# Kernel tuning notes

Measured on AMD Instinct MI355X. Metric: run time of the kernel, lower is better.

The kernel has to match this reference:

```python
import jax, jax.numpy as jnp
import numpy as np

B, S, H = 1, 4096, 2048
NH, HD = 16, 128  # num_heads, head_dim = H // NH


def setup_inputs() -> dict:
    key = jax.random.key(0)
    k1, k2, k3 = jax.random.split(key, 3)
    x = jax.random.normal(k1, (B, S, H), dtype=jnp.float32)
    w_qkv = jax.random.normal(k2, (3 * H, H), dtype=jnp.float32) * (1.0 / np.sqrt(H))
    w_out = jax.random.normal(k3, (H, H), dtype=jnp.float32) * (1.0 / np.sqrt(H))
    return {"x": x, "w_qkv": w_qkv, "w_out": w_out}


def reference(x, w_qkv, w_out):
    b, s, _ = x.shape
    # qkv projection: torch Linear computes x @ W^T
    qkv = jnp.einsum('bsh,oh->bso', x, w_qkv)
    qkv = qkv.reshape(b, s, 3, NH, HD).transpose(2, 0, 3, 1, 4)  # [3,B,NH,S,HD]
    q, k, v = qkv[0], qkv[1], qkv[2]
    # world_size == 1 -> single ring step == full attention with online softmax
    scores = jnp.einsum('bhqd,bhkd->bhqk', q, k) / np.sqrt(HD)
    m = jnp.max(scores, axis=-1, keepdims=True)          # running max (single step)
    p = jnp.exp(scores - m)                              # scores_exp
    out = jnp.einsum('bhqk,bhkd->bhqd', p, v)
    denom = jnp.sum(p, axis=-1, keepdims=True) + 1e-8    # running_sum + eps
    out = out / denom
    out = out.transpose(0, 2, 1, 3).reshape(b, s, H)     # [B,S,H]
    return jnp.einsum('bsh,oh->bso', out, w_out)
```

## Files before the change

kernel.cpp:

```cpp
#include <hip/hip_runtime.h>
#include <stdint.h>

typedef __attribute__((ext_vector_type(4))) float f32x4;
typedef __attribute__((ext_vector_type(16))) float f32x16;
typedef __attribute__((ext_vector_type(8))) short bf16x8;
typedef unsigned short u16;

#define MFMA(a, b, c) __builtin_amdgcn_mfma_f32_16x16x32_bf16(a, b, c, 0, 0, 0)
#define MFMA32(a, b, c) __builtin_amdgcn_mfma_f32_32x32x16_bf16(a, b, c, 0, 0, 0)
#define EXP2(x) __builtin_amdgcn_exp2f(x)
#define FENCE asm volatile("" ::: "memory")
#define BARRIER do { FENCE; __builtin_amdgcn_s_barrier(); FENCE; } while (0)

__device__ __forceinline__ u16 f2bf(float f) {
  union { float f; unsigned u; } x; x.f = f;
  unsigned r = x.u + 0x7fffu + ((x.u >> 16) & 1u);
  return (u16)(r >> 16);
}

__device__ __forceinline__ unsigned cvtpk(float lo, float hi) {
  unsigned r;
  asm("v_cvt_pk_bf16_f32 %0, %1, %2" : "=v"(r) : "v"(lo), "v"(hi));
  return r;
}

__device__ __forceinline__ void pl32swap(unsigned& a, unsigned& b) {
  asm volatile("v_permlane32_swap_b32 %0, %1" : "+v"(a), "+v"(b));
}

__device__ __forceinline__ void gload16(const void* g, void* l) {
  __builtin_amdgcn_global_load_lds(
      (const __attribute__((address_space(1))) unsigned int*)g,
      (__attribute__((address_space(3))) unsigned int*)l, 16, 0, 0);
}

__global__ void __launch_bounds__(256)
cast_all(const float* __restrict__ x, const float* __restrict__ wq,
         const float* __restrict__ wo, u16* __restrict__ xb,
         u16* __restrict__ wqb, u16* __restrict__ wob) {
  for (int idx = blockIdx.x * 256 + threadIdx.x; idx < 6291456; idx += 256 * 2048) {
    const float* in;
    u16* out;
    int j;
    if (idx < 2097152) { in = x; out = xb; j = idx; }
    else if (idx < 5242880) { in = wq; out = wqb; j = idx - 2097152; }
    else { in = wo; out = wob; j = idx - 5242880; }
    float4 v = reinterpret_cast<const float4*>(in)[j];
    ushort4 o;
    o.x = f2bf(v.x); o.y = f2bf(v.y); o.z = f2bf(v.z); o.w = f2bf(v.w);
    reinterpret_cast<ushort4*>(out)[j] = o;
  }
}

template <int EPI>
__global__ void __launch_bounds__(512)
gemm8(const u16* __restrict__ A, const u16* __restrict__ B,
      void* __restrict__ C0, void* __restrict__ C1, void* __restrict__ C2,
      int M, int N, int K, int MBt) {
  __shared__ alignas(16) char smb[98304];
  const int tid = threadIdx.x;
  const int w = tid >> 6, lane = tid & 63;
  const int lr = lane & 15, g = lane >> 4;
  const int wm = w >> 2, wn = w & 3;
  const int gb = (blockIdx.x & 7) * ((int)gridDim.x >> 3) + (blockIdx.x >> 3);
  const int mb = gb % MBt, nb = gb / MBt;
  const int m0 = mb * 128, n0 = nb * 256;
  const int NT = K >> 6, NIT = NT >> 1;

  const int l8 = lane >> 3, l7 = lane & 7;
  const int csb = (l7 ^ l8) * 16;
  const char* asrc;
  unsigned adst;
  {
    int r = (w & 3) * 8 + ((w >> 2) << 6) + l8;
    asrc = (const char*)(A + (size_t)(m0 + r) * K) + csb;
    adst = (unsigned)(r * 128 + l7 * 16);
  }
  const char* bsrcb[2];
  unsigned bdst[2];
#pragma unroll
  for (int j = 0; j < 2; ++j) {
    int c = 2 * w + j;
    int r = (c & 3) * 8 + ((c >> 2) << 6) + l8;
    bsrcb[j] = (const char*)(B + (size_t)(n0 + r) * K) + csb;
    bdst[j] = (unsigned)(r * 128 + l7 * 16);
  }
  const size_t row32 = (size_t)32 * K * 2;

#define STG(kt, u)                                                               \
  do {                                                                           \
    if ((kt) < NT) {                                                             \
      size_t _ko = (size_t)(kt) * 128;                                           \
      int _da = ((kt) & 1) ? 16384 : 0;                                          \
      int _db = 32768 + (((kt) & 1) ? 32768 : 0);                                \
      if ((u) == 0) {                                                            \
        gload16(asrc + _ko, smb + _da + adst);                                   \
      } else if ((u) == 1) {                                                     \
        gload16(bsrcb[0] + _ko, smb + _db + bdst[0]);                            \
        gload16(bsrcb[1] + _ko, smb + _db + bdst[1]);                            \
      } else if ((u) == 2) {                                                     \
        gload16(asrc + row32 + _ko, smb + _da + 4096 + adst);                    \
      } else {                                                                   \
        gload16(bsrcb[0] + row32 + _ko, smb + _db + 4096 + bdst[0]);             \
        gload16(bsrcb[1] + row32 + _ko, smb + _db + 4096 + bdst[1]);             \
      }                                                                          \
    }                                                                            \
  } while (0)
#define VMC(n) asm volatile("s_waitcnt vmcnt(" #n ")" ::: "memory")

  f32x4 acc[4][4];
#pragma unroll
  for (int x = 0; x < 4; ++x)
#pragma unroll
    for (int y = 0; y < 4; ++y) acc[x][y] = f32x4{0.f, 0.f, 0.f, 0.f};
  bf16x8 af[2][2], bf01[2][2], bf23[2][2];
  const int aoff0 = ((g) ^ (lr & 7)) << 4;
  const int aoff1 = ((4 + g) ^ (lr & 7)) << 4;
  const int arowb = (wm * 64 + lr) * 128;
  const int browb = (wn * 64 + lr) * 128;

  auto LDA = [&](const char* base, int mih) {
#pragma unroll
    for (int mi = 0; mi < 2; ++mi) {
      const char* p = base + arowb + (mih * 32 + mi * 16) * 128;
      af[mi][0] = *(const bf16x8*)(p + aoff0);
      af[mi][1] = *(const bf16x8*)(p + aoff1);
    }
  };
  auto LDB = [&](const char* base, bf16x8 (*bfr)[2], int nih) {
#pragma unroll
    for (int ni = 0; ni < 2; ++ni) {
      const char* p = base + browb + (nih * 32 + ni * 16) * 128;
      bfr[ni][0] = *(const bf16x8*)(p + aoff0);
      bfr[ni][1] = *(const bf16x8*)(p + aoff1);
    }
  };
  auto MM = [&](int mih, int nih, bf16x8 (*bfr)[2]) {
#pragma unroll
    for (int mi = 0; mi < 2; ++mi)
#pragma unroll
      for (int ni = 0; ni < 2; ++ni) {
        acc[mih * 2 + mi][nih * 2 + ni] =
            MFMA(af[mi][0], bfr[ni][0], acc[mih * 2 + mi][nih * 2 + ni]);
        acc[mih * 2 + mi][nih * 2 + ni] =
            MFMA(af[mi][1], bfr[ni][1], acc[mih * 2 + mi][nih * 2 + ni]);
      }
  };

  STG(0, 0); STG(0, 1); STG(0, 2); STG(0, 3);
  STG(1, 0); STG(1, 1); STG(1, 3);
  VMC(5);
  BARRIER;

  const char* A0 = smb;
  const char* A1 = smb + 16384;
  const char* B0 = smb + 32768;
  const char* B1 = smb + 65536;

  for (int it = 0; it < NIT; ++it) {
    const int t0 = 2 * it;
    const bool last = (it == NIT - 1);
    LDA(A0, 0); LDB(B0, bf01, 0); LDB(B0, bf23, 1);
    STG(t0 + 1, 2);
    VMC(6);
    BARRIER;
    __builtin_amdgcn_s_setprio(1); MM(0, 0, bf01); MM(0, 1, bf23); __builtin_amdgcn_s_setprio(0);
    BARRIER;
    LDA(A0, 1);
    STG(t0 + 2, 0); STG(t0 + 2, 1); STG(t0 + 2, 3);
    if (last) VMC(1); else VMC(6);
    BARRIER;
    __builtin_amdgcn_s_setprio(1); MM(1, 1, bf23); MM(1, 0, bf01); __builtin_amdgcn_s_setprio(0);
    BARRIER;
    LDA(A1, 0); LDB(B1, bf01, 0); LDB(B1, bf23, 1);
    STG(t0 + 2, 2);
    if (last) VMC(0); else VMC(6);
    BARRIER;
    __builtin_amdgcn_s_setprio(1); MM(0, 0, bf01); MM(0, 1, bf23); __builtin_amdgcn_s_setprio(0);
    BARRIER;
    LDA(A1, 1);
    STG(t0 + 3, 0); STG(t0 + 3, 1); STG(t0 + 3, 3);
    if (last) VMC(0); else VMC(6);
    BARRIER;
    __builtin_amdgcn_s_setprio(1); MM(1, 1, bf23); MM(1, 0, bf01); __builtin_amdgcn_s_setprio(0);
    BARRIER;
  }
#undef STG
#undef VMC

  if (EPI == 0) {
    const float qs = 0.08838834764831845f * 1.4426950408889634f;
    u16* qo = (u16*)C0;
    u16* ko = (u16*)C1;
    u16* vo = (u16*)C2;
#pragma unroll
    for (int a = 0; a < 4; ++a) {
      int s0 = m0 + wm * 64 + a * 16 + g * 4;
#pragma unroll
      for (int b = 0; b < 4; ++b) {
        int n = n0 + wn * 64 + b * 16 + lr;
        int t = n >> 11, hh = (n >> 7) & 15, d = n & 127;
        if (t == 2) {
          ushort4 pk;
          pk.x = f2bf(acc[a][b][0]);
          pk.y = f2bf(acc[a][b][1]);
          pk.z = f2bf(acc[a][b][2]);
          pk.w = f2bf(acc[a][b][3]);
          *(ushort4*)(vo + (size_t)(hh * 128 + d) * 4096 + s0) = pk;
        } else {
          float sc = (t == 0) ? qs : 1.f;
          u16* dq = (t == 0 ? qo : ko) + (size_t)(hh * 4096 + s0) * 128 + d;
#pragma unroll
          for (int j = 0; j < 4; ++j) dq[(size_t)j * 128] = f2bf(acc[a][b][j] * sc);
        }
      }
    }
  } else {
    float* C = (float*)C0;
#pragma unroll
    for (int a = 0; a < 4; ++a)
#pragma unroll
      for (int b = 0; b < 4; ++b) {
        size_t r0 = (size_t)(m0 + wm * 64 + a * 16 + g * 4);
        int cn = n0 + wn * 64 + b * 16 + lr;
#pragma unroll
        for (int j = 0; j < 4; ++j) C[(r0 + j) * N + cn] = acc[a][b][j];
      }
  }
}

__global__ void __launch_bounds__(512)
attn_kernel(const u16* __restrict__ qg, const u16* __restrict__ kg,
            const u16* __restrict__ vtg, u16* __restrict__ og) {
  __shared__ alignas(64) char smb[131072];
  const int tid = threadIdx.x;
  const int w = tid >> 6, lane = tid & 63;
  const int ql = lane & 31, hl = lane >> 5;
  const int gb = (blockIdx.x & 7) * 32 + (blockIdx.x >> 3);
  const int h = gb >> 4;
  const int qb = gb & 15;

  const u16* ssrc[8];
  unsigned sdst[8];
  size_t sstep;
  if (w < 4) {
    sstep = 128 * 128;
#pragma unroll
    for (int i = 0; i < 8; ++i) {
      int c = w * 8 + i;
      int r = c * 4 + (lane >> 4);
      int sb = (lane & 15) ^ (r & 15);
      ssrc[i] = kg + (size_t)(h * 4096 + r) * 128 + sb * 8;
      sdst[i] = c * 1024;
    }
  } else {
    sstep = 128;
#pragma unroll
    for (int i = 0; i < 8; ++i) {
      int c = (w - 4) * 8 + i;
      int r = c * 4 + (lane >> 4);
      int sb = (lane & 15) ^ (r & 15);
      ssrc[i] = vtg + (size_t)(h * 128 + r) * 4096 + sb * 8;
      sdst[i] = 65536 + c * 1024;
    }
  }

  const u16* qrow = qg + (size_t)(h * 4096 + qb * 256 + w * 32 + ql) * 128 + hl * 8;
  bf16x8 qf[8];
#pragma unroll
  for (int s = 0; s < 8; ++s) qf[s] = *(const bf16x8*)(qrow + s * 16);

  f32x16 of[4];
#pragma unroll
  for (int i = 0; i < 4; ++i)
#pragma unroll
    for (int r = 0; r < 16; ++r) of[i][r] = 0.f;
  float mrun = -1e30f, lsum = 0.f;
  const float thr = 6.0f;

#pragma unroll
  for (int i = 0; i < 8; ++i) gload16(ssrc[i], smb + sdst[i]);

  const int kxor = (ql & 15) << 4;
  for (int t = 0; t < 32; ++t) {
    const int cur = t & 1;
    asm volatile("s_waitcnt vmcnt(0)" ::: "memory");
    __builtin_amdgcn_s_barrier();
    FENCE;
    if (t + 1 < 32) {
      const int nb = (t + 1) & 1;
#pragma unroll
      for (int i = 0; i < 8; ++i)
        gload16(ssrc[i] + (size_t)(t + 1) * sstep, smb + sdst[i] + nb * 32768);
    }
    const char* kbuf = smb + cur * 32768;
    const char* vbuf = smb + 65536 + cur * 32768;

    f32x16 st[4];
#pragma unroll
    for (int kb = 0; kb < 4; ++kb)
#pragma unroll
      for (int r = 0; r < 16; ++r) st[kb][r] = 0.f;
    __builtin_amdgcn_s_setprio(1);
#pragma unroll
    for (int s = 0; s < 8; ++s) {
      int off = ((s * 2 + hl) << 4) ^ kxor;
      bf16x8 k0 = *(const bf16x8*)(kbuf + (0 * 32 + ql) * 256 + off);
      bf16x8 k1 = *(const bf16x8*)(kbuf + (1 * 32 + ql) * 256 + off);
      bf16x8 k2 = *(const bf16x8*)(kbuf + (2 * 32 + ql) * 256 + off);
      bf16x8 k3 = *(const bf16x8*)(kbuf + (3 * 32 + ql) * 256 + off);
      st[0] = MFMA32(k0, qf[s], st[0]);
      st[1] = MFMA32(k1, qf[s], st[1]);
      st[2] = MFMA32(k2, qf[s], st[2]);
      st[3] = MFMA32(k3, qf[s], st[3]);
    }
    __builtin_amdgcn_s_setprio(0);

    float tmax = -1e30f;
#pragma unroll
    for (int kb = 0; kb < 4; ++kb)
#pragma unroll
      for (int r = 0; r < 16; ++r) tmax = fmaxf(tmax, st[kb][r]);
    tmax = fmaxf(tmax, __shfl_xor(tmax, 32));
    if (!__all(tmax - mrun <= thr)) {
      float mnew = fmaxf(mrun, tmax);
      float esc = EXP2(mrun - mnew);
#pragma unroll
      for (int db = 0; db < 4; ++db)
#pragma unroll
        for (int r = 0; r < 16; ++r) of[db][r] *= esc;
      lsum *= esc;
      mrun = mnew;
    }
    float psum = 0.f;
    union U { unsigned u[4]; bf16x8 v; };
    U paf[8];
#pragma unroll
    for (int gp = 0; gp < 2; ++gp) {
      unsigned pk0[8], pk1[8];
#pragma unroll
      for (int i = 0; i < 8; ++i) {
        float a0 = EXP2(st[2 * gp + 0][2 * i] - mrun);
        float b0 = EXP2(st[2 * gp + 0][2 * i + 1] - mrun);
        float a1 = EXP2(st[2 * gp + 1][2 * i] - mrun);
        float b1 = EXP2(st[2 * gp + 1][2 * i + 1] - mrun);
        psum += (a0 + b0) + (a1 + b1);
        pk0[i] = cvtpk(a0, b0);
        pk1[i] = cvtpk(a1, b1);
      }
      pl32swap(pk0[0], pk0[2]); pl32swap(pk0[1], pk0[3]);
      pl32swap(pk0[4], pk0[6]); pl32swap(pk0[5], pk0[7]);
      pl32swap(pk1[0], pk1[2]); pl32swap(pk1[1], pk1[3]);
      pl32swap(pk1[4], pk1[6]); pl32swap(pk1[5], pk1[7]);
#pragma unroll
      for (int i = 0; i < 4; ++i) {
        paf[gp * 4 + 0].u[i] = pk0[i];
        paf[gp * 4 + 1].u[i] = pk0[4 + i];
        paf[gp * 4 + 2].u[i] = pk1[i];
        paf[gp * 4 + 3].u[i] = pk1[4 + i];
      }
    }
    psum += __shfl_xor(psum, 32);
    lsum += psum;

    __builtin_amdgcn_s_setprio(1);
#pragma unroll
    for (int db = 0; db < 4; ++db) {
      const char* vrow = vbuf + (db * 32 + ql) * 256;
#pragma unroll
      for (int kp = 0; kp < 8; ++kp) {
        int m = (kp * 2 + hl) ^ (ql & 15);
        bf16x8 vf = *(const bf16x8*)(vrow + m * 16);
        of[db] = MFMA32(vf, paf[kp].v, of[db]);
      }
    }
    __builtin_amdgcn_s_setprio(0);
    FENCE;
  }

  float linv = 1.f / (lsum + 1e-8f);
  size_t qrow_o = (size_t)(qb * 256 + w * 32 + ql) * 2048 + h * 128;
#pragma unroll
  for (int db = 0; db < 4; ++db)
#pragma unroll
    for (int u = 0; u < 4; ++u) {
      ushort4 pk;
      pk.x = f2bf(of[db][4 * u + 0] * linv);
      pk.y = f2bf(of[db][4 * u + 1] * linv);
      pk.z = f2bf(of[db][4 * u + 2] * linv);
      pk.w = f2bf(of[db][4 * u + 3] * linv);
      *(ushort4*)(og + qrow_o + db * 32 + 8 * u + hl * 4) = pk;
    }
}

extern "C" void kernel_launch(void* const* d_in, const int* in_sizes, int n_in,
                              void* d_out, int out_size, void* d_ws, size_t ws_size,
                              hipStream_t stream) {
  const float* x = (const float*)d_in[0];
  const float* w_qkv = (const float*)d_in[1];
  const float* w_out = (const float*)d_in[2];

  char* ws = (char*)d_ws;
  u16* xb = (u16*)(ws + 0);
  u16* wqkvb = (u16*)(ws + 16777216);
  u16* woutb = (u16*)(ws + 41943040);
  u16* qb = (u16*)(ws + 50331648);
  u16* kb = (u16*)(ws + 67108864);
  u16* vtb = (u16*)(ws + 83886080);
  u16* aob = (u16*)(ws + 100663296);

  cast_all<<<2048, 256, 0, stream>>>(x, w_qkv, w_out, xb, wqkvb, woutb);
  gemm8<0><<<768, 512, 0, stream>>>(xb, wqkvb, qb, kb, vtb, 4096, 6144, 2048, 32);
  attn_kernel<<<256, 512, 0, stream>>>(qb, kb, vtb, aob);
  gemm8<1><<<256, 512, 0, stream>>>(aob, woutb, d_out, nullptr, nullptr, 4096, 2048, 2048, 32);
}
```

Baseline: 312.3 us.

## Split attention KV range across two wave groups and combine partials in LDS

The attention kernel now handles 128 queries per block with two groups of four waves, each group covering half of the KV sequence, so the grid doubles to 512 blocks. LDS drops to about 66 KB so two blocks can share a CU, and the partial outputs and softmax statistics of the two groups are merged through LDS at the end. The K/V double buffering is replaced by a single buffer with load-then-wait between barriers. This gives up copy/compute overlap inside a block and relies on co-resident blocks to hide load latency. It also adds an epilogue merge step.

```diff
diff --git a/kernel.cpp b/kernel.cpp
--- a/kernel.cpp
+++ b/kernel.cpp
@@ -232,40 +232,47 @@
 __global__ void __launch_bounds__(512)
 attn_kernel(const u16* __restrict__ qg, const u16* __restrict__ kg,
             const u16* __restrict__ vtg, u16* __restrict__ og) {
-  __shared__ alignas(64) char smb[131072];
+  __shared__ alignas(64) char smb[67584];
   const int tid = threadIdx.x;
   const int w = tid >> 6, lane = tid & 63;
   const int ql = lane & 31, hl = lane >> 5;
-  const int gb = (blockIdx.x & 7) * 32 + (blockIdx.x >> 3);
-  const int h = gb >> 4;
-  const int qb = gb & 15;
+  const int gb = (blockIdx.x & 7) * 64 + (blockIdx.x >> 3);
+  const int h = gb >> 5;
+  const int qb = gb & 31;
+  const int g2 = w >> 2;
+  const int qw = w & 3;
 
   const u16* ssrc[8];
   unsigned sdst[8];
   size_t sstep;
-  if (w < 4) {
-    sstep = 128 * 128;
-#pragma unroll
-    for (int i = 0; i < 8; ++i) {
-      int c = w * 8 + i;
-      int r = c * 4 + (lane >> 4);
-      int sb = (lane & 15) ^ (r & 15);
-      ssrc[i] = kg + (size_t)(h * 4096 + r) * 128 + sb * 8;
-      sdst[i] = c * 1024;
-    }
-  } else {
-    sstep = 128;
-#pragma unroll
-    for (int i = 0; i < 8; ++i) {
-      int c = (w - 4) * 8 + i;
-      int r = c * 4 + (lane >> 4);
-      int sb = (lane & 15) ^ (r & 15);
-      ssrc[i] = vtg + (size_t)(h * 128 + r) * 4096 + sb * 8;
-      sdst[i] = 65536 + c * 1024;
-    }
-  }
-
-  const u16* qrow = qg + (size_t)(h * 4096 + qb * 256 + w * 32 + ql) * 128 + hl * 8;
+  {
+    const int u = w >> 1;
+    const int sg = u >> 1;
+    if (!(u & 1)) {
+      sstep = 64 * 128;
+#pragma unroll
+      for (int i = 0; i < 8; ++i) {
+        int c = (w & 1) * 8 + i;
+        int r = c * 4 + (lane >> 4);
+        int sb = (lane & 15) ^ (r & 15);
+        ssrc[i] = kg + (size_t)(h * 4096 + sg * 2048 + r) * 128 + sb * 8;
+        sdst[i] = sg * 16384 + c * 1024;
+      }
+    } else {
+      sstep = 64;
+#pragma unroll
+      for (int i = 0; i < 8; ++i) {
+        int c = (w & 1) * 8 + i;
+        int j = c * 4 + (lane >> 4);
+        int x = (lane & 15) ^ (j & 15);
+        int e = x >> 3, b = x & 7;
+        ssrc[i] = vtg + (size_t)(h * 128 + 2 * j + e) * 4096 + sg * 2048 + b * 8;
+        sdst[i] = 32768 + sg * 16384 + c * 1024;
+      }
+    }
+  }
+
+  const u16* qrow = qg + (size_t)(h * 4096 + qb * 128 + qw * 32 + ql) * 128 + hl * 8;
   bf16x8 qf[8];
 #pragma unroll
   for (int s = 0; s < 8; ++s) qf[s] = *(const bf16x8*)(qrow + s * 16);
@@ -278,49 +285,35 @@
   float mrun = -1e30f, lsum = 0.f;
   const float thr = 6.0f;
 
+  const int kxor = (ql & 15) << 4;
+  const char* kbuf = smb + g2 * 16384;
+  const char* vbuf = smb + 32768 + g2 * 16384;
+  const int vj = ql >> 1;
+  const int ve8 = (ql & 1) << 3;
+
 #pragma unroll
   for (int i = 0; i < 8; ++i) gload16(ssrc[i], smb + sdst[i]);
-
-  const int kxor = (ql & 15) << 4;
+  asm volatile("s_waitcnt vmcnt(0)" ::: "memory");
+  BARRIER;
+
   for (int t = 0; t < 32; ++t) {
-    const int cur = t & 1;
-    asm volatile("s_waitcnt vmcnt(0)" ::: "memory");
-    __builtin_amdgcn_s_barrier();
-    FENCE;
-    if (t + 1 < 32) {
-      const int nb = (t + 1) & 1;
-#pragma unroll
-      for (int i = 0; i < 8; ++i)
-        gload16(ssrc[i] + (size_t)(t + 1) * sstep, smb + sdst[i] + nb * 32768);
-    }
-    const char* kbuf = smb + cur * 32768;
-    const char* vbuf = smb + 65536 + cur * 32768;
-
-    f32x16 st[4];
-#pragma unroll
-    for (int kb = 0; kb < 4; ++kb)
-#pragma unroll
-      for (int r = 0; r < 16; ++r) st[kb][r] = 0.f;
+    f32x16 st0, st1;
+#pragma unroll
+    for (int r = 0; r < 16; ++r) { st0[r] = 0.f; st1[r] = 0.f; }
     __builtin_amdgcn_s_setprio(1);
 #pragma unroll
     for (int s = 0; s < 8; ++s) {
       int off = ((s * 2 + hl) << 4) ^ kxor;
-      bf16x8 k0 = *(const bf16x8*)(kbuf + (0 * 32 + ql) * 256 + off);
-      bf16x8 k1 = *(const bf16x8*)(kbuf + (1 * 32 + ql) * 256 + off);
-      bf16x8 k2 = *(const bf16x8*)(kbuf + (2 * 32 + ql) * 256 + off);
-      bf16x8 k3 = *(const bf16x8*)(kbuf + (3 * 32 + ql) * 256 + off);
-      st[0] = MFMA32(k0, qf[s], st[0]);
-      st[1] = MFMA32(k1, qf[s], st[1]);
-      st[2] = MFMA32(k2, qf[s], st[2]);
-      st[3] = MFMA32(k3, qf[s], st[3]);
+      bf16x8 k0 = *(const bf16x8*)(kbuf + ql * 256 + off);
+      bf16x8 k1 = *(const bf16x8*)(kbuf + (32 + ql) * 256 + off);
+      st0 = MFMA32(k0, qf[s], st0);
+      st1 = MFMA32(k1, qf[s], st1);
     }
     __builtin_amdgcn_s_setprio(0);
 
     float tmax = -1e30f;
 #pragma unroll
-    for (int kb = 0; kb < 4; ++kb)
-#pragma unroll
-      for (int r = 0; r < 16; ++r) tmax = fmaxf(tmax, st[kb][r]);
+    for (int r = 0; r < 16; ++r) tmax = fmaxf(tmax, fmaxf(st0[r], st1[r]));
     tmax = fmaxf(tmax, __shfl_xor(tmax, 32));
     if (!__all(tmax - mrun <= thr)) {
       float mnew = fmaxf(mrun, tmax);
@@ -333,64 +326,89 @@
       mrun = mnew;
     }
     float psum = 0.f;
-    union U { unsigned u[4]; bf16x8 v; };
-    U paf[8];
-#pragma unroll
-    for (int gp = 0; gp < 2; ++gp) {
-      unsigned pk0[8], pk1[8];
-#pragma unroll
-      for (int i = 0; i < 8; ++i) {
-        float a0 = EXP2(st[2 * gp + 0][2 * i] - mrun);
-        float b0 = EXP2(st[2 * gp + 0][2 * i + 1] - mrun);
-        float a1 = EXP2(st[2 * gp + 1][2 * i] - mrun);
-        float b1 = EXP2(st[2 * gp + 1][2 * i + 1] - mrun);
-        psum += (a0 + b0) + (a1 + b1);
-        pk0[i] = cvtpk(a0, b0);
-        pk1[i] = cvtpk(a1, b1);
-      }
-      pl32swap(pk0[0], pk0[2]); pl32swap(pk0[1], pk0[3]);
-      pl32swap(pk0[4], pk0[6]); pl32swap(pk0[5], pk0[7]);
-      pl32swap(pk1[0], pk1[2]); pl32swap(pk1[1], pk1[3]);
-      pl32swap(pk1[4], pk1[6]); pl32swap(pk1[5], pk1[7]);
-#pragma unroll
-      for (int i = 0; i < 4; ++i) {
-        paf[gp * 4 + 0].u[i] = pk0[i];
-        paf[gp * 4 + 1].u[i] = pk0[4 + i];
-        paf[gp * 4 + 2].u[i] = pk1[i];
-        paf[gp * 4 + 3].u[i] = pk1[4 + i];
-      }
+    unsigned pk0[8], pk1[8];
+#pragma unroll
+    for (int i = 0; i < 8; ++i) {
+      float a0 = EXP2(st0[2 * i] - mrun);
+      float b0 = EXP2(st0[2 * i + 1] - mrun);
+      float a1 = EXP2(st1[2 * i] - mrun);
+      float b1 = EXP2(st1[2 * i + 1] - mrun);
+      psum += (a0 + b0) + (a1 + b1);
+      pk0[i] = cvtpk(a0, b0);
+      pk1[i] = cvtpk(a1, b1);
     }
     psum += __shfl_xor(psum, 32);
     lsum += psum;
 
+    pl32swap(pk0[0], pk0[2]); pl32swap(pk0[1], pk0[3]);
+    pl32swap(pk0[4], pk0[6]); pl32swap(pk0[5], pk0[7]);
+    pl32swap(pk1[0], pk1[2]); pl32swap(pk1[1], pk1[3]);
+    pl32swap(pk1[4], pk1[6]); pl32swap(pk1[5], pk1[7]);
+    union U { unsigned u[4]; bf16x8 v; };
+    U paf[4];
+#pragma unroll
+    for (int i = 0; i < 4; ++i) { paf[0].u[i] = pk0[i]; paf[1].u[i] = pk0[4 + i]; }
+#pragma unroll
+    for (int i = 0; i < 4; ++i) { paf[2].u[i] = pk1[i]; paf[3].u[i] = pk1[4 + i]; }
+
     __builtin_amdgcn_s_setprio(1);
 #pragma unroll
     for (int db = 0; db < 4; ++db) {
-      const char* vrow = vbuf + (db * 32 + ql) * 256;
-#pragma unroll
-      for (int kp = 0; kp < 8; ++kp) {
-        int m = (kp * 2 + hl) ^ (ql & 15);
+      int j = db * 16 + vj;
+      const char* vrow = vbuf + j * 256;
+#pragma unroll
+      for (int kp = 0; kp < 4; ++kp) {
+        int m = (ve8 | (kp * 2 + hl)) ^ (j & 15);
         bf16x8 vf = *(const bf16x8*)(vrow + m * 16);
         of[db] = MFMA32(vf, paf[kp].v, of[db]);
       }
     }
     __builtin_amdgcn_s_setprio(0);
-    FENCE;
-  }
-
-  float linv = 1.f / (lsum + 1e-8f);
-  size_t qrow_o = (size_t)(qb * 256 + w * 32 + ql) * 2048 + h * 128;
-#pragma unroll
-  for (int db = 0; db < 4; ++db)
-#pragma unroll
-    for (int u = 0; u < 4; ++u) {
-      ushort4 pk;
-      pk.x = f2bf(of[db][4 * u + 0] * linv);
-      pk.y = f2bf(of[db][4 * u + 1] * linv);
-      pk.z = f2bf(of[db][4 * u + 2] * linv);
-      pk.w = f2bf(of[db][4 * u + 3] * linv);
-      *(ushort4*)(og + qrow_o + db * 32 + 8 * u + hl * 4) = pk;
-    }
+
+    BARRIER;
+    if (t + 1 < 32) {
+#pragma unroll
+      for (int i = 0; i < 8; ++i)
+        gload16(ssrc[i] + (size_t)(t + 1) * sstep, smb + sdst[i]);
+      asm volatile("s_waitcnt vmcnt(0)" ::: "memory");
+    }
+    BARRIER;
+  }
+
+  __syncthreads();
+  if (w >= 4) {
+    char* base = smb + qw * 16384 + lane * 256;
+#pragma unroll
+    for (int db = 0; db < 4; ++db) *(f32x16*)(base + db * 64) = of[db];
+    float2 ml;
+    ml.x = mrun; ml.y = lsum;
+    *(float2*)(smb + 65536 + (qw * 64 + lane) * 8) = ml;
+  }
+  __syncthreads();
+  if (w < 4) {
+    const char* base = smb + qw * 16384 + lane * 256;
+    float2 ml = *(const float2*)(smb + 65536 + (qw * 64 + lane) * 8);
+    float m = fmaxf(mrun, ml.x);
+    float a0 = EXP2(mrun - m);
+    float a1 = EXP2(ml.x - m);
+    float l = lsum * a0 + ml.y * a1;
+    float linv = 1.f / (l + 1e-8f);
+    float fa0 = a0 * linv, fa1 = a1 * linv;
+    size_t qrow_o = (size_t)(qb * 128 + qw * 32 + ql) * 2048 + h * 128;
+#pragma unroll
+    for (int db = 0; db < 4; ++db) {
+      f32x16 ob = *(const f32x16*)(base + db * 64);
+#pragma unroll
+      for (int u = 0; u < 4; ++u) {
+        ushort4 pk;
+        pk.x = f2bf(of[db][4 * u + 0] * fa0 + ob[4 * u + 0] * fa1);
+        pk.y = f2bf(of[db][4 * u + 1] * fa0 + ob[4 * u + 1] * fa1);
+        pk.z = f2bf(of[db][4 * u + 2] * fa0 + ob[4 * u + 2] * fa1);
+        pk.w = f2bf(of[db][4 * u + 3] * fa0 + ob[4 * u + 3] * fa1);
+        *(ushort4*)(og + qrow_o + db * 32 + 8 * u + hl * 4) = pk;
+      }
+    }
+  }
 }
 
 extern "C" void kernel_launch(void* const* d_in, const int* in_sizes, int n_in,
@@ -411,6 +429,6 @@
 
   cast_all<<<2048, 256, 0, stream>>>(x, w_qkv, w_out, xb, wqkvb, woutb);
   gemm8<0><<<768, 512, 0, stream>>>(xb, wqkvb, qb, kb, vtb, 4096, 6144, 2048, 32);
-  attn_kernel<<<256, 512, 0, stream>>>(qb, kb, vtb, aob);
+  attn_kernel<<<512, 512, 0, stream>>>(qb, kb, vtb, aob);
   gemm8<1><<<256, 512, 0, stream>>>(aob, woutb, d_out, nullptr, nullptr, 4096, 2048, 2048, 32);
 }
```

Result: slower. 360.0 us (+15.3%).
